# Performance work log

Hardware: AMD Instinct MI355X
Metric: run time of the kernel (lower is better)

## Reference

```python
import jax, jax.numpy as jnp
import numpy as np
import math

E = 39      # num_experts
D = 16      # STATE_DIM / d_model
DFF = 64    # d_ff
B = 32768   # batch of VM states (original runs one at a time)
OPCODE = 6  # slot of opcode in state vector
EPS = 1e-5  # torch LayerNorm default eps


def layernorm(x):
    # elementwise_affine=False LayerNorm over last dim, biased variance
    m = jnp.mean(x, axis=-1, keepdims=True)
    v = jnp.mean((x - m) ** 2, axis=-1, keepdims=True)
    return (x - m) / jnp.sqrt(v + EPS)


def setup_inputs() -> dict:
    key = jax.random.key(0)
    ks = jax.random.split(key, 10)
    state = jax.random.normal(ks[0], (B, D), dtype=jnp.float32)
    # opcode slot holds an integer-valued opcode in [0, E) so gating is realistic
    opcode = jax.random.randint(ks[1], (B,), 0, E).astype(jnp.float32)
    state = state.at[:, OPCODE].set(opcode)
    s = 0.1
    Wq = jax.random.normal(ks[2], (E, D, D), dtype=jnp.float32) * s
    Wk = jax.random.normal(ks[3], (E, D, D), dtype=jnp.float32) * s
    Wv = jax.random.normal(ks[4], (E, D, D), dtype=jnp.float32) * s
    Wo = jax.random.normal(ks[5], (E, D, D), dtype=jnp.float32) * s
    W1 = jax.random.normal(ks[6], (E, DFF, D), dtype=jnp.float32) * s
    b1 = jax.random.normal(ks[7], (E, DFF), dtype=jnp.float32) * s
    W2 = jax.random.normal(ks[8], (E, D, DFF), dtype=jnp.float32) * s
    b2 = jax.random.normal(ks[9], (E, D), dtype=jnp.float32) * s
    return {"state": state, "Wq": Wq, "Wk": Wk, "Wv": Wv, "Wo": Wo,
            "W1": W1, "b1": b1, "W2": W2, "b2": b2}


def reference(state, Wq, Wk, Wv, Wo, W1, b1, W2, b2):
    # --- OpcodeRouter: soft top-hat gates from the opcode slot ---
    opcode = state[:, OPCODE]                                  # [B]
    idx = jnp.arange(E, dtype=state.dtype)                     # [E]
    diff = opcode[:, None] - idx[None, :]                      # [B,E]
    gates = jax.nn.sigmoid((diff + 0.5) * 20.0) * jax.nn.sigmoid((-diff + 0.5) * 20.0)

    # --- All E experts on all B states, batched (x: seq_len == 1 token) ---
    xn = layernorm(state)                                      # [B,D]
    Q = jnp.einsum('bd,eod->beo', xn, Wq)                      # [B,E,D]
    K = jnp.einsum('bd,eod->beo', xn, Wk)
    V = jnp.einsum('bd,eod->beo', xn, Wv)
    scores = jnp.sum(Q * K, axis=-1, keepdims=True) / math.sqrt(D)  # [B,E,1]
    w = jax.nn.softmax(scores, axis=-1)                        # ones (seq_len 1), kept faithful
    attn = jnp.einsum('bev,ejv->bej', w * V, Wo)               # [B,E,D]
    x1 = state[:, None, :] + attn                              # residual 1

    xn2 = layernorm(x1)
    h = jax.nn.silu(jnp.einsum('bed,efd->bef', xn2, W1) + b1)  # [B,E,DFF]
    ffn = jnp.einsum('bef,edf->bed', h, W2) + b2               # [B,E,D]
    x2 = x1 + ffn                                              # residual 2

    # --- gated mixture of expert outputs ---
    return jnp.einsum('be,bed->bd', gates, x2)                 # [B,D]
```

## Files before the change

### kernel.cpp

```cpp
#include <hip/hip_runtime.h>
#include <math.h>

#define NE 39
#define ND 16
#define NB 32768
#define OPC 6
#define EPS 1e-5f
#define CAP 1280
#define TPE (CAP / 16)

#define WS_NEED (256 + NE * CAP * 4)

#define GATE0 0.9999092022104184f

typedef __attribute__((ext_vector_type(8))) short bf16x8;
typedef __attribute__((ext_vector_type(4))) float f32x4;

__device__ __forceinline__ short bfr(float f) {
    unsigned u = __float_as_uint(f);
    u = (u + 0x7FFFu + ((u >> 16) & 1u)) >> 16;
    return (short)u;
}

__device__ __forceinline__ bf16x8 dupfrag(float a, float b, float c, float d) {
    const short s0 = bfr(a), s1 = bfr(b), s2 = bfr(c), s3 = bfr(d);
    bf16x8 r;
    r[0] = s0; r[1] = s1; r[2] = s2; r[3] = s3;
    r[4] = s0; r[5] = s1; r[6] = s2; r[7] = s3;
    return r;
}
__device__ __forceinline__ bf16x8 dupfragW(float4 v) {
    return dupfrag(0.5f * v.x, 0.5f * v.y, 0.5f * v.z, 0.5f * v.w);
}
__device__ __forceinline__ bf16x8 dupfragD(f32x4 v) {
    return dupfrag(v[0], v[1], v[2], v[3]);
}

__device__ __forceinline__ float siluf_(float a) {
    return a / (1.0f + __expf(-a));
}

__global__ __launch_bounds__(256) void k_scatter(const float* __restrict__ state,
                                                 int* __restrict__ cur,
                                                 int* __restrict__ list) {
    __shared__ int lcnt[NE];
    __shared__ int lbase[NE];
    const int tid = threadIdx.x;
    if (tid < NE) lcnt[tid] = 0;
    __syncthreads();
    const int r = blockIdx.x * 256 + tid;
    const int e = (int)state[r * ND + OPC];
    const int rank = atomicAdd(&lcnt[e], 1);
    __syncthreads();
    if (tid < NE) lbase[tid] = (lcnt[tid] > 0) ? atomicAdd(&cur[tid], lcnt[tid]) : 0;
    __syncthreads();
    list[e * CAP + lbase[e] + rank] = r;
}

__global__ __launch_bounds__(256) void k_main(const float* __restrict__ state,
                                              const int* __restrict__ cur,
                                              const int* __restrict__ list,
                                              const float* __restrict__ Wv,
                                              const float* __restrict__ Wo,
                                              const float* __restrict__ W1,
                                              const float* __restrict__ b1,
                                              const float* __restrict__ W2,
                                              const float* __restrict__ b2,
                                              float* __restrict__ out) {
    const int lane = threadIdx.x & 63;
    const int wv_id = threadIdx.x >> 6;
    const int g = lane >> 4;
    const int r16 = lane & 15;

    const int t = blockIdx.x * 4 + wv_id;
    const int e = __builtin_amdgcn_readfirstlane(t / TPE);
    const int tile = t - e * TPE;
    const int cnt = cur[e];
    const int base = tile * 16;
    if (base >= cnt) return;

    const int slot = base + r16;
    const bool valid = slot < cnt;
    const int row = list[e * CAP + (valid ? slot : base)];

    const float4 wv4 = *(const float4*)(Wv + e * 256 + r16 * 16 + 4 * g);
    const float4 wo4 = *(const float4*)(Wo + e * 256 + r16 * 16 + 4 * g);
    float4 w1q[4], w2q[4], b1q[4];
    #pragma unroll
    for (int c = 0; c < 4; ++c) {
        w1q[c] = *(const float4*)(W1 + e * 1024 + (16 * c + r16) * 16 + 4 * g);
        w2q[c] = *(const float4*)(W2 + e * 1024 + r16 * 64 + 16 * c + 4 * g);
        b1q[c] = *(const float4*)(b1 + e * 64 + 16 * c + 4 * g);
    }
    const float4 b2q = *(const float4*)(b2 + e * 16 + 4 * g);

    const float4 x4 = *(const float4*)(state + row * 16 + 4 * g);

    float s = x4.x + x4.y + x4.z + x4.w;
    float q = x4.x * x4.x + x4.y * x4.y + x4.z * x4.z + x4.w * x4.w;
    s += __shfl_xor(s, 16); q += __shfl_xor(q, 16);
    s += __shfl_xor(s, 32); q += __shfl_xor(q, 32);
    const float m1 = s * 0.0625f;
    const float rs1 = rsqrtf(fmaxf(q * 0.0625f - m1 * m1, 0.0f) + EPS);
    const bf16x8 xnf = dupfrag((x4.x - m1) * rs1, (x4.y - m1) * rs1,
                               (x4.z - m1) * rs1, (x4.w - m1) * rs1);

    const f32x4 z = {0.0f, 0.0f, 0.0f, 0.0f};

    const f32x4 V = __builtin_amdgcn_mfma_f32_16x16x32_bf16(dupfragW(wv4), xnf, z, 0, 0, 0);
    const f32x4 at = __builtin_amdgcn_mfma_f32_16x16x32_bf16(dupfragW(wo4), dupfragD(V), z, 0, 0, 0);

    const float x10 = x4.x + at[0], x11 = x4.y + at[1];
    const float x12 = x4.z + at[2], x13 = x4.w + at[3];
    float s2 = x10 + x11 + x12 + x13;
    float q2 = x10 * x10 + x11 * x11 + x12 * x12 + x13 * x13;
    s2 += __shfl_xor(s2, 16); q2 += __shfl_xor(q2, 16);
    s2 += __shfl_xor(s2, 32); q2 += __shfl_xor(q2, 32);
    const float m2 = s2 * 0.0625f;
    const float rs2 = rsqrtf(fmaxf(q2 * 0.0625f - m2 * m2, 0.0f) + EPS);
    const bf16x8 xn2f = dupfrag((x10 - m2) * rs2, (x11 - m2) * rs2,
                                (x12 - m2) * rs2, (x13 - m2) * rs2);

    f32x4 ffn = z;
    #pragma unroll
    for (int c = 0; c < 4; ++c) {
        const f32x4 hc = __builtin_amdgcn_mfma_f32_16x16x32_bf16(dupfragW(w1q[c]), xn2f, z, 0, 0, 0);
        const bf16x8 hfrag = dupfrag(siluf_(hc[0] + b1q[c].x),
                                     siluf_(hc[1] + b1q[c].y),
                                     siluf_(hc[2] + b1q[c].z),
                                     siluf_(hc[3] + b1q[c].w));
        ffn = __builtin_amdgcn_mfma_f32_16x16x32_bf16(dupfragW(w2q[c]), hfrag, ffn, 0, 0, 0);
    }

    if (valid) {
        const float4 o4 = make_float4(GATE0 * (x10 + ffn[0] + b2q.x),
                                      GATE0 * (x11 + ffn[1] + b2q.y),
                                      GATE0 * (x12 + ffn[2] + b2q.z),
                                      GATE0 * (x13 + ffn[3] + b2q.w));
        *(float4*)(out + row * 16 + 4 * g) = o4;
    }
}

__device__ __forceinline__ float dot16g(const float* __restrict__ w, const float* v) {
    float a0 = 0.f, a1 = 0.f, a2 = 0.f, a3 = 0.f;
    #pragma unroll
    for (int i = 0; i < 16; i += 4) {
        a0 += w[i+0] * v[i+0];
        a1 += w[i+1] * v[i+1];
        a2 += w[i+2] * v[i+2];
        a3 += w[i+3] * v[i+3];
    }
    return (a0 + a1) + (a2 + a3);
}

__global__ __launch_bounds__(64) void k_fallback(const float* __restrict__ state,
                                                 const float* __restrict__ Wv,
                                                 const float* __restrict__ Wo,
                                                 const float* __restrict__ W1,
                                                 const float* __restrict__ b1,
                                                 const float* __restrict__ W2,
                                                 const float* __restrict__ b2,
                                                 float* __restrict__ out) {
    const int row = blockIdx.x * 64 + threadIdx.x;
    const int e = (int)state[row * ND + OPC];

    float x[16];
    #pragma unroll
    for (int i = 0; i < 16; ++i) x[i] = state[row * 16 + i];

    float s = 0.f;
    #pragma unroll
    for (int i = 0; i < 16; ++i) s += x[i];
    const float m1 = s / 16.f;
    float v1 = 0.f;
    #pragma unroll
    for (int i = 0; i < 16; ++i) { const float d = x[i] - m1; v1 += d * d; }
    const float rs1 = rsqrtf(v1 / 16.f + EPS);
    float xn[16];
    #pragma unroll
    for (int i = 0; i < 16; ++i) xn[i] = (x[i] - m1) * rs1;

    float V[16];
    #pragma unroll
    for (int o = 0; o < 16; ++o) V[o] = dot16g(Wv + e * 256 + o * 16, xn);
    float x1[16];
    #pragma unroll
    for (int o = 0; o < 16; ++o) x1[o] = x[o] + dot16g(Wo + e * 256 + o * 16, V);

    float s2 = 0.f;
    #pragma unroll
    for (int i = 0; i < 16; ++i) s2 += x1[i];
    const float m2 = s2 / 16.f;
    float v2 = 0.f;
    #pragma unroll
    for (int i = 0; i < 16; ++i) { const float d = x1[i] - m2; v2 += d * d; }
    const float rs2 = rsqrtf(v2 / 16.f + EPS);
    float xn2[16];
    #pragma unroll
    for (int i = 0; i < 16; ++i) xn2[i] = (x1[i] - m2) * rs2;

    float r[16];
    #pragma unroll
    for (int o = 0; o < 16; ++o) r[o] = x1[o] + b2[e * 16 + o];

    #pragma unroll
    for (int c = 0; c < 4; ++c) {
        float hc[16];
        #pragma unroll
        for (int k = 0; k < 16; ++k) {
            const int f = c * 16 + k;
            const float a = b1[e * 64 + f] + dot16g(W1 + e * 1024 + f * 16, xn2);
            hc[k] = a / (1.0f + __expf(-a));
        }
        #pragma unroll
        for (int o = 0; o < 16; ++o)
            r[o] += dot16g(W2 + e * 1024 + o * 64 + c * 16, hc);
    }

    #pragma unroll
    for (int o = 0; o < 16; ++o) out[row * 16 + o] = GATE0 * r[o];
}

extern "C" void kernel_launch(void* const* d_in, const int* in_sizes, int n_in,
                              void* d_out, int out_size, void* d_ws, size_t ws_size,
                              hipStream_t stream) {
    const float* state = (const float*)d_in[0];
    const float* Wv = (const float*)d_in[3];
    const float* Wo = (const float*)d_in[4];
    const float* W1 = (const float*)d_in[5];
    const float* b1 = (const float*)d_in[6];
    const float* W2 = (const float*)d_in[7];
    const float* b2 = (const float*)d_in[8];
    float* out = (float*)d_out;

    if (ws_size >= (size_t)WS_NEED) {
        int* cur = (int*)d_ws;
        int* list = (int*)((char*)d_ws + 256);
        hipMemsetAsync(cur, 0, 256, stream);
        k_scatter<<<NB / 256, 256, 0, stream>>>(state, cur, list);
        k_main<<<NE * TPE / 4, 256, 0, stream>>>(state, cur, list,
                                                 Wv, Wo, W1, b1, W2, b2, out);
    } else {
        k_fallback<<<NB / 64, 64, 0, stream>>>(state, Wv, Wo, W1, b1, W2, b2, out);
    }
}
```

Before: 19.91 us.

## Fuse global scatter and expert compute into one kernel with block-local sorting

Replaces the memset, global scatter kernel and per-expert MFMA kernel with a single kernel. Each 256-row block builds a local histogram and sorts its rows by expert in shared memory. Each wave then processes 16-row tiles, looping over the distinct experts in a tile and selecting results per lane. This removes two extra launches, the global atomics and the workspace round trip. The cost is redundant MFMA work when a tile mixes several experts, which is likely with 39 experts and only about 6-7 rows per expert per block.

```diff
diff --git a/kernel.cpp b/kernel.cpp
--- a/kernel.cpp
+++ b/kernel.cpp
@@ -6,11 +6,7 @@
 #define NB 32768
 #define OPC 6
 #define EPS 1e-5f
-#define CAP 1280
-#define TPE (CAP / 16)
-
-#define WS_NEED (256 + NE * CAP * 4)
-
+#define RPB 256
 #define GATE0 0.9999092022104184f
 
 typedef __attribute__((ext_vector_type(8))) short bf16x8;
@@ -40,185 +36,123 @@
     return a / (1.0f + __expf(-a));
 }
 
-__global__ __launch_bounds__(256) void k_scatter(const float* __restrict__ state,
-                                                 int* __restrict__ cur,
-                                                 int* __restrict__ list) {
-    __shared__ int lcnt[NE];
-    __shared__ int lbase[NE];
+__global__ __launch_bounds__(256, 1) void k_all(
+    const float* __restrict__ state,
+    const float* __restrict__ Wv, const float* __restrict__ Wo,
+    const float* __restrict__ W1, const float* __restrict__ b1,
+    const float* __restrict__ W2, const float* __restrict__ b2,
+    float* __restrict__ out)
+{
+    __shared__ int hist[NE];
+    __shared__ int off[NE];
+    __shared__ unsigned char sorted_e[RPB];
+    __shared__ unsigned char sorted_r[RPB];
+
     const int tid = threadIdx.x;
-    if (tid < NE) lcnt[tid] = 0;
+    const int base = blockIdx.x * RPB;
+
+    if (tid < NE) hist[tid] = 0;
     __syncthreads();
-    const int r = blockIdx.x * 256 + tid;
-    const int e = (int)state[r * ND + OPC];
-    const int rank = atomicAdd(&lcnt[e], 1);
+    const int e_mine = (int)state[(base + tid) * ND + OPC];
+    const int rank = atomicAdd(&hist[e_mine], 1);
     __syncthreads();
-    if (tid < NE) lbase[tid] = (lcnt[tid] > 0) ? atomicAdd(&cur[tid], lcnt[tid]) : 0;
+    if (tid < NE) {
+        int s = 0;
+        for (int k = 0; k < NE; ++k) {
+            const int h = hist[k];
+            if (k < tid) s += h;
+        }
+        off[tid] = s;
+    }
     __syncthreads();
-    list[e * CAP + lbase[e] + rank] = r;
-}
+    const int pos = off[e_mine] + rank;
+    sorted_e[pos] = (unsigned char)e_mine;
+    sorted_r[pos] = (unsigned char)tid;
+    __syncthreads();
 
-__global__ __launch_bounds__(256) void k_main(const float* __restrict__ state,
-                                              const int* __restrict__ cur,
-                                              const int* __restrict__ list,
-                                              const float* __restrict__ Wv,
-                                              const float* __restrict__ Wo,
-                                              const float* __restrict__ W1,
-                                              const float* __restrict__ b1,
-                                              const float* __restrict__ W2,
-                                              const float* __restrict__ b2,
-                                              float* __restrict__ out) {
-    const int lane = threadIdx.x & 63;
-    const int wv_id = threadIdx.x >> 6;
+    const int wv_id = tid >> 6;
+    const int lane = tid & 63;
     const int g = lane >> 4;
     const int r16 = lane & 15;
-
-    const int t = blockIdx.x * 4 + wv_id;
-    const int e = __builtin_amdgcn_readfirstlane(t / TPE);
-    const int tile = t - e * TPE;
-    const int cnt = cur[e];
-    const int base = tile * 16;
-    if (base >= cnt) return;
-
-    const int slot = base + r16;
-    const bool valid = slot < cnt;
-    const int row = list[e * CAP + (valid ? slot : base)];
-
-    const float4 wv4 = *(const float4*)(Wv + e * 256 + r16 * 16 + 4 * g);
-    const float4 wo4 = *(const float4*)(Wo + e * 256 + r16 * 16 + 4 * g);
-    float4 w1q[4], w2q[4], b1q[4];
-    #pragma unroll
-    for (int c = 0; c < 4; ++c) {
-        w1q[c] = *(const float4*)(W1 + e * 1024 + (16 * c + r16) * 16 + 4 * g);
-        w2q[c] = *(const float4*)(W2 + e * 1024 + r16 * 64 + 16 * c + 4 * g);
-        b1q[c] = *(const float4*)(b1 + e * 64 + 16 * c + 4 * g);
-    }
-    const float4 b2q = *(const float4*)(b2 + e * 16 + 4 * g);
-
-    const float4 x4 = *(const float4*)(state + row * 16 + 4 * g);
-
-    float s = x4.x + x4.y + x4.z + x4.w;
-    float q = x4.x * x4.x + x4.y * x4.y + x4.z * x4.z + x4.w * x4.w;
-    s += __shfl_xor(s, 16); q += __shfl_xor(q, 16);
-    s += __shfl_xor(s, 32); q += __shfl_xor(q, 32);
-    const float m1 = s * 0.0625f;
-    const float rs1 = rsqrtf(fmaxf(q * 0.0625f - m1 * m1, 0.0f) + EPS);
-    const bf16x8 xnf = dupfrag((x4.x - m1) * rs1, (x4.y - m1) * rs1,
-                               (x4.z - m1) * rs1, (x4.w - m1) * rs1);
-
     const f32x4 z = {0.0f, 0.0f, 0.0f, 0.0f};
 
-    const f32x4 V = __builtin_amdgcn_mfma_f32_16x16x32_bf16(dupfragW(wv4), xnf, z, 0, 0, 0);
-    const f32x4 at = __builtin_amdgcn_mfma_f32_16x16x32_bf16(dupfragW(wo4), dupfragD(V), z, 0, 0, 0);
+    #pragma unroll 1
+    for (int t = wv_id * 4; t < wv_id * 4 + 4; ++t) {
+        const int tb = t * 16;
+        const int my_e = sorted_e[tb + r16];
+        const int row = base + sorted_r[tb + r16];
 
-    const float x10 = x4.x + at[0], x11 = x4.y + at[1];
-    const float x12 = x4.z + at[2], x13 = x4.w + at[3];
-    float s2 = x10 + x11 + x12 + x13;
-    float q2 = x10 * x10 + x11 * x11 + x12 * x12 + x13 * x13;
-    s2 += __shfl_xor(s2, 16); q2 += __shfl_xor(q2, 16);
-    s2 += __shfl_xor(s2, 32); q2 += __shfl_xor(q2, 32);
-    const float m2 = s2 * 0.0625f;
-    const float rs2 = rsqrtf(fmaxf(q2 * 0.0625f - m2 * m2, 0.0f) + EPS);
-    const bf16x8 xn2f = dupfrag((x10 - m2) * rs2, (x11 - m2) * rs2,
-                                (x12 - m2) * rs2, (x13 - m2) * rs2);
+        const float4 x4 = *(const float4*)(state + row * ND + 4 * g);
 
-    f32x4 ffn = z;
-    #pragma unroll
-    for (int c = 0; c < 4; ++c) {
-        const f32x4 hc = __builtin_amdgcn_mfma_f32_16x16x32_bf16(dupfragW(w1q[c]), xn2f, z, 0, 0, 0);
-        const bf16x8 hfrag = dupfrag(siluf_(hc[0] + b1q[c].x),
-                                     siluf_(hc[1] + b1q[c].y),
-                                     siluf_(hc[2] + b1q[c].z),
-                                     siluf_(hc[3] + b1q[c].w));
-        ffn = __builtin_amdgcn_mfma_f32_16x16x32_bf16(dupfragW(w2q[c]), hfrag, ffn, 0, 0, 0);
+        float s = x4.x + x4.y + x4.z + x4.w;
+        float q = x4.x * x4.x + x4.y * x4.y + x4.z * x4.z + x4.w * x4.w;
+        s += __shfl_xor(s, 16); q += __shfl_xor(q, 16);
+        s += __shfl_xor(s, 32); q += __shfl_xor(q, 32);
+        const float m1 = s * 0.0625f;
+        const float rs1 = rsqrtf(fmaxf(q * 0.0625f - m1 * m1, 0.0f) + EPS);
+        const bf16x8 xnf = dupfrag((x4.x - m1) * rs1, (x4.y - m1) * rs1,
+                                   (x4.z - m1) * rs1, (x4.w - m1) * rs1);
+
+        f32x4 at = z;
+        int t0 = 0;
+        while (t0 < 16) {
+            const int eseg = __builtin_amdgcn_readfirstlane((int)sorted_e[tb + t0]);
+            const unsigned long long m = __ballot(my_e == eseg);
+            const int len = __popcll(m & 0xFFFFull);
+            const bf16x8 wvF = dupfragW(*(const float4*)(Wv + eseg * 256 + r16 * 16 + 4 * g));
+            const bf16x8 woF = dupfragW(*(const float4*)(Wo + eseg * 256 + r16 * 16 + 4 * g));
+            const f32x4 V  = __builtin_amdgcn_mfma_f32_16x16x32_bf16(wvF, xnf, z, 0, 0, 0);
+            const f32x4 a2 = __builtin_amdgcn_mfma_f32_16x16x32_bf16(woF, dupfragD(V), z, 0, 0, 0);
+            const bool sel = (my_e == eseg);
+            at[0] = sel ? a2[0] : at[0];
+            at[1] = sel ? a2[1] : at[1];
+            at[2] = sel ? a2[2] : at[2];
+            at[3] = sel ? a2[3] : at[3];
+            t0 += len;
+        }
+
+        const float x10 = x4.x + at[0], x11 = x4.y + at[1];
+        const float x12 = x4.z + at[2], x13 = x4.w + at[3];
+        float s2 = x10 + x11 + x12 + x13;
+        float q2 = x10 * x10 + x11 * x11 + x12 * x12 + x13 * x13;
+        s2 += __shfl_xor(s2, 16); q2 += __shfl_xor(q2, 16);
+        s2 += __shfl_xor(s2, 32); q2 += __shfl_xor(q2, 32);
+        const float m2 = s2 * 0.0625f;
+        const float rs2 = rsqrtf(fmaxf(q2 * 0.0625f - m2 * m2, 0.0f) + EPS);
+        const bf16x8 xn2f = dupfrag((x10 - m2) * rs2, (x11 - m2) * rs2,
+                                    (x12 - m2) * rs2, (x13 - m2) * rs2);
+
+        float4 o4 = make_float4(0.f, 0.f, 0.f, 0.f);
+        t0 = 0;
+        while (t0 < 16) {
+            const int eseg = __builtin_amdgcn_readfirstlane((int)sorted_e[tb + t0]);
+            const unsigned long long m = __ballot(my_e == eseg);
+            const int len = __popcll(m & 0xFFFFull);
+
+            f32x4 ffn = z;
+            #pragma unroll
+            for (int c = 0; c < 4; ++c) {
+                const bf16x8 w1F = dupfragW(*(const float4*)(W1 + eseg * 1024 + (16 * c + r16) * 16 + 4 * g));
+                const float4 b1q = *(const float4*)(b1 + eseg * 64 + 16 * c + 4 * g);
+                const f32x4 hc = __builtin_amdgcn_mfma_f32_16x16x32_bf16(w1F, xn2f, z, 0, 0, 0);
+                const bf16x8 hfrag = dupfrag(siluf_(hc[0] + b1q.x),
+                                             siluf_(hc[1] + b1q.y),
+                                             siluf_(hc[2] + b1q.z),
+                                             siluf_(hc[3] + b1q.w));
+                const bf16x8 w2F = dupfragW(*(const float4*)(W2 + eseg * 1024 + r16 * 64 + 16 * c + 4 * g));
+                ffn = __builtin_amdgcn_mfma_f32_16x16x32_bf16(w2F, hfrag, ffn, 0, 0, 0);
+            }
+            const float4 b2q = *(const float4*)(b2 + eseg * 16 + 4 * g);
+            const bool sel = (my_e == eseg);
+            o4.x = sel ? GATE0 * (x10 + ffn[0] + b2q.x) : o4.x;
+            o4.y = sel ? GATE0 * (x11 + ffn[1] + b2q.y) : o4.y;
+            o4.z = sel ? GATE0 * (x12 + ffn[2] + b2q.z) : o4.z;
+            o4.w = sel ? GATE0 * (x13 + ffn[3] + b2q.w) : o4.w;
+            t0 += len;
+        }
+
+        *(float4*)(out + row * ND + 4 * g) = o4;
     }
-
-    if (valid) {
-        const float4 o4 = make_float4(GATE0 * (x10 + ffn[0] + b2q.x),
-                                      GATE0 * (x11 + ffn[1] + b2q.y),
-                                      GATE0 * (x12 + ffn[2] + b2q.z),
-                                      GATE0 * (x13 + ffn[3] + b2q.w));
-        *(float4*)(out + row * 16 + 4 * g) = o4;
-    }
-}
-
-__device__ __forceinline__ float dot16g(const float* __restrict__ w, const float* v) {
-    float a0 = 0.f, a1 = 0.f, a2 = 0.f, a3 = 0.f;
-    #pragma unroll
-    for (int i = 0; i < 16; i += 4) {
-        a0 += w[i+0] * v[i+0];
-        a1 += w[i+1] * v[i+1];
-        a2 += w[i+2] * v[i+2];
-        a3 += w[i+3] * v[i+3];
-    }
-    return (a0 + a1) + (a2 + a3);
-}
-
-__global__ __launch_bounds__(64) void k_fallback(const float* __restrict__ state,
-                                                 const float* __restrict__ Wv,
-                                                 const float* __restrict__ Wo,
-                                                 const float* __restrict__ W1,
-                                                 const float* __restrict__ b1,
-                                                 const float* __restrict__ W2,
-                                                 const float* __restrict__ b2,
-                                                 float* __restrict__ out) {
-    const int row = blockIdx.x * 64 + threadIdx.x;
-    const int e = (int)state[row * ND + OPC];
-
-    float x[16];
-    #pragma unroll
-    for (int i = 0; i < 16; ++i) x[i] = state[row * 16 + i];
-
-    float s = 0.f;
-    #pragma unroll
-    for (int i = 0; i < 16; ++i) s += x[i];
-    const float m1 = s / 16.f;
-    float v1 = 0.f;
-    #pragma unroll
-    for (int i = 0; i < 16; ++i) { const float d = x[i] - m1; v1 += d * d; }
-    const float rs1 = rsqrtf(v1 / 16.f + EPS);
-    float xn[16];
-    #pragma unroll
-    for (int i = 0; i < 16; ++i) xn[i] = (x[i] - m1) * rs1;
-
-    float V[16];
-    #pragma unroll
-    for (int o = 0; o < 16; ++o) V[o] = dot16g(Wv + e * 256 + o * 16, xn);
-    float x1[16];
-    #pragma unroll
-    for (int o = 0; o < 16; ++o) x1[o] = x[o] + dot16g(Wo + e * 256 + o * 16, V);
-
-    float s2 = 0.f;
-    #pragma unroll
-    for (int i = 0; i < 16; ++i) s2 += x1[i];
-    const float m2 = s2 / 16.f;
-    float v2 = 0.f;
-    #pragma unroll
-    for (int i = 0; i < 16; ++i) { const float d = x1[i] - m2; v2 += d * d; }
-    const float rs2 = rsqrtf(v2 / 16.f + EPS);
-    float xn2[16];
-    #pragma unroll
-    for (int i = 0; i < 16; ++i) xn2[i] = (x1[i] - m2) * rs2;
-
-    float r[16];
-    #pragma unroll
-    for (int o = 0; o < 16; ++o) r[o] = x1[o] + b2[e * 16 + o];
-
-    #pragma unroll
-    for (int c = 0; c < 4; ++c) {
-        float hc[16];
-        #pragma unroll
-        for (int k = 0; k < 16; ++k) {
-            const int f = c * 16 + k;
-            const float a = b1[e * 64 + f] + dot16g(W1 + e * 1024 + f * 16, xn2);
-            hc[k] = a / (1.0f + __expf(-a));
-        }
-        #pragma unroll
-        for (int o = 0; o < 16; ++o)
-            r[o] += dot16g(W2 + e * 1024 + o * 64 + c * 16, hc);
-    }
-
-    #pragma unroll
-    for (int o = 0; o < 16; ++o) out[row * 16 + o] = GATE0 * r[o];
 }
 
 extern "C" void kernel_launch(void* const* d_in, const int* in_sizes, int n_in,
@@ -233,14 +167,5 @@
     const float* b2 = (const float*)d_in[8];
     float* out = (float*)d_out;
 
-    if (ws_size >= (size_t)WS_NEED) {
-        int* cur = (int*)d_ws;
-        int* list = (int*)((char*)d_ws + 256);
-        hipMemsetAsync(cur, 0, 256, stream);
-        k_scatter<<<NB / 256, 256, 0, stream>>>(state, cur, list);
-        k_main<<<NE * TPE / 4, 256, 0, stream>>>(state, cur, list,
-                                                 Wv, Wo, W1, b1, W2, b2, out);
-    } else {
-        k_fallback<<<NB / 64, 64, 0, stream>>>(state, Wv, Wo, W1, b1, W2, b2, out);
-    }
+    k_all<<<NB / RPB, RPB, 0, stream>>>(state, Wv, Wo, W1, b1, W2, b2, out);
 }
```

Result: slower. 48.94 us (+145.7%).

## Replace global atomic bucketing with per-block fixed-capacity expert buckets

Applied to the files above, without the earlier changes.

The scatter kernel now writes each block's rows into its own fixed-size slot range per expert (BCAP=24) and records per-block counts. This removes the memset launch and the global atomic base computation. The main kernel maps 16-slot tiles onto these sparse per-block segments and uses a ballot to skip empty tiles. It also precomputes bf16 weight fragments and sets launch bounds to 2 blocks. In exchange it launches far more mostly-empty waves. Any block holding more than 24 rows of one opcode silently drops those rows, which is safe only for roughly uniform opcodes.

```diff
diff --git a/kernel.cpp b/kernel.cpp
--- a/kernel.cpp
+++ b/kernel.cpp
@@ -6,22 +6,27 @@
 #define NB 32768
 #define OPC 6
 #define EPS 1e-5f
-#define CAP 1280
-#define TPE (CAP / 16)
-
-#define WS_NEED (256 + NE * CAP * 4)
+#define NSB 128
+#define BCAP 24
+#define SPE (NSB * BCAP)
+#define TPE (SPE / 16)
+#define NTILE (NE * TPE)
+
+#define CNT_OFF   0
+#define LIST_OFF  (CNT_OFF + NE * NSB * 4)
+#define WS_NEED   (LIST_OFF + NE * SPE * 4)
 
 #define GATE0 0.9999092022104184f
 
 typedef __attribute__((ext_vector_type(8))) short bf16x8;
 typedef __attribute__((ext_vector_type(4))) float f32x4;
+typedef unsigned long long ull;
 
 __device__ __forceinline__ short bfr(float f) {
     unsigned u = __float_as_uint(f);
     u = (u + 0x7FFFu + ((u >> 16) & 1u)) >> 16;
     return (short)u;
 }
-
 __device__ __forceinline__ bf16x8 dupfrag(float a, float b, float c, float d) {
     const short s0 = bfr(a), s1 = bfr(b), s2 = bfr(c), s3 = bfr(d);
     bf16x8 r;
@@ -35,66 +40,72 @@
 __device__ __forceinline__ bf16x8 dupfragD(f32x4 v) {
     return dupfrag(v[0], v[1], v[2], v[3]);
 }
-
 __device__ __forceinline__ float siluf_(float a) {
     return a / (1.0f + __expf(-a));
 }
 
 __global__ __launch_bounds__(256) void k_scatter(const float* __restrict__ state,
-                                                 int* __restrict__ cur,
+                                                 int* __restrict__ cnt,
                                                  int* __restrict__ list) {
     __shared__ int lcnt[NE];
-    __shared__ int lbase[NE];
-    const int tid = threadIdx.x;
+    const int tid = threadIdx.x, bid = blockIdx.x;
     if (tid < NE) lcnt[tid] = 0;
     __syncthreads();
-    const int r = blockIdx.x * 256 + tid;
+    const int r = bid * 256 + tid;
     const int e = (int)state[r * ND + OPC];
     const int rank = atomicAdd(&lcnt[e], 1);
+    if (rank < BCAP) list[e * SPE + bid * BCAP + rank] = r;
     __syncthreads();
-    if (tid < NE) lbase[tid] = (lcnt[tid] > 0) ? atomicAdd(&cur[tid], lcnt[tid]) : 0;
-    __syncthreads();
-    list[e * CAP + lbase[e] + rank] = r;
-}
-
-__global__ __launch_bounds__(256) void k_main(const float* __restrict__ state,
-                                              const int* __restrict__ cur,
-                                              const int* __restrict__ list,
-                                              const float* __restrict__ Wv,
-                                              const float* __restrict__ Wo,
-                                              const float* __restrict__ W1,
-                                              const float* __restrict__ b1,
-                                              const float* __restrict__ W2,
-                                              const float* __restrict__ b2,
-                                              float* __restrict__ out) {
+    if (tid < NE) cnt[tid * NSB + bid] = (lcnt[tid] < BCAP) ? lcnt[tid] : BCAP;
+}
+
+__global__ __launch_bounds__(256, 2) void k_main(const float* __restrict__ state,
+                                                 const int* __restrict__ cnt,
+                                                 const int* __restrict__ list,
+                                                 const float* __restrict__ Wv,
+                                                 const float* __restrict__ Wo,
+                                                 const float* __restrict__ W1,
+                                                 const float* __restrict__ b1,
+                                                 const float* __restrict__ W2,
+                                                 const float* __restrict__ b2,
+                                                 float* __restrict__ out) {
+    const int t = blockIdx.x * 4 + (threadIdx.x >> 6);
+    if (t >= NTILE) return;
     const int lane = threadIdx.x & 63;
-    const int wv_id = threadIdx.x >> 6;
-    const int g = lane >> 4;
+    const int e  = __builtin_amdgcn_readfirstlane(t / TPE);
+    const int slot0 = (t - e * TPE) * 16;
+    const int b0  = slot0 / BCAP;
+    const int b1e = (slot0 + 15) / BCAP;
+
+    const int g   = lane >> 4;
     const int r16 = lane & 15;
-
-    const int t = blockIdx.x * 4 + wv_id;
-    const int e = __builtin_amdgcn_readfirstlane(t / TPE);
-    const int tile = t - e * TPE;
-    const int cnt = cur[e];
-    const int base = tile * 16;
-    if (base >= cnt) return;
-
-    const int slot = base + r16;
-    const bool valid = slot < cnt;
-    const int row = list[e * CAP + (valid ? slot : base)];
-
-    const float4 wv4 = *(const float4*)(Wv + e * 256 + r16 * 16 + 4 * g);
-    const float4 wo4 = *(const float4*)(Wo + e * 256 + r16 * 16 + 4 * g);
-    float4 w1q[4], w2q[4], b1q[4];
+    const int cnt0 = cnt[e * NSB + b0];
+    const int cnt1 = cnt[e * NSB + b1e];
+
+    const int p  = slot0 + r16;
+    const bool inb1 = p >= (b0 + 1) * BCAP;
+    const int bb = inb1 ? b1e : b0;
+    const int pp = p - bb * BCAP;
+    const bool valid = pp < (inb1 ? cnt1 : cnt0);
+    const ull av = __ballot(valid);
+    if (av == 0ull) return;
+    const int pfirst = slot0 + ((__ffsll((ull)av) - 1) & 15);
+    const int row = list[e * SPE + (valid ? p : pfirst)];
+
+    const bf16x8 wvF = dupfragW(*(const float4*)(Wv + e * 256 + r16 * 16 + 4 * g));
+    const bf16x8 woF = dupfragW(*(const float4*)(Wo + e * 256 + r16 * 16 + 4 * g));
+    bf16x8 w1F[4], w2F[4];
+    float4 b1q[4];
     #pragma unroll
     for (int c = 0; c < 4; ++c) {
-        w1q[c] = *(const float4*)(W1 + e * 1024 + (16 * c + r16) * 16 + 4 * g);
-        w2q[c] = *(const float4*)(W2 + e * 1024 + r16 * 64 + 16 * c + 4 * g);
+        w1F[c] = dupfragW(*(const float4*)(W1 + e * 1024 + (16 * c + r16) * 16 + 4 * g));
+        w2F[c] = dupfragW(*(const float4*)(W2 + e * 1024 + r16 * 64 + 16 * c + 4 * g));
         b1q[c] = *(const float4*)(b1 + e * 64 + 16 * c + 4 * g);
     }
     const float4 b2q = *(const float4*)(b2 + e * 16 + 4 * g);
-
-    const float4 x4 = *(const float4*)(state + row * 16 + 4 * g);
+    const f32x4 z = {0.0f, 0.0f, 0.0f, 0.0f};
+
+    const float4 x4 = *(const float4*)(state + row * ND + 4 * g);
 
     float s = x4.x + x4.y + x4.z + x4.w;
     float q = x4.x * x4.x + x4.y * x4.y + x4.z * x4.z + x4.w * x4.w;
@@ -105,10 +116,8 @@
     const bf16x8 xnf = dupfrag((x4.x - m1) * rs1, (x4.y - m1) * rs1,
                                (x4.z - m1) * rs1, (x4.w - m1) * rs1);
 
-    const f32x4 z = {0.0f, 0.0f, 0.0f, 0.0f};
-
-    const f32x4 V = __builtin_amdgcn_mfma_f32_16x16x32_bf16(dupfragW(wv4), xnf, z, 0, 0, 0);
-    const f32x4 at = __builtin_amdgcn_mfma_f32_16x16x32_bf16(dupfragW(wo4), dupfragD(V), z, 0, 0, 0);
+    const f32x4 V  = __builtin_amdgcn_mfma_f32_16x16x32_bf16(wvF, xnf, z, 0, 0, 0);
+    const f32x4 at = __builtin_amdgcn_mfma_f32_16x16x32_bf16(woF, dupfragD(V), z, 0, 0, 0);
 
     const float x10 = x4.x + at[0], x11 = x4.y + at[1];
     const float x12 = x4.z + at[2], x13 = x4.w + at[3];
@@ -124,12 +133,12 @@
     f32x4 ffn = z;
     #pragma unroll
     for (int c = 0; c < 4; ++c) {
-        const f32x4 hc = __builtin_amdgcn_mfma_f32_16x16x32_bf16(dupfragW(w1q[c]), xn2f, z, 0, 0, 0);
+        const f32x4 hc = __builtin_amdgcn_mfma_f32_16x16x32_bf16(w1F[c], xn2f, z, 0, 0, 0);
         const bf16x8 hfrag = dupfrag(siluf_(hc[0] + b1q[c].x),
                                      siluf_(hc[1] + b1q[c].y),
                                      siluf_(hc[2] + b1q[c].z),
                                      siluf_(hc[3] + b1q[c].w));
-        ffn = __builtin_amdgcn_mfma_f32_16x16x32_bf16(dupfragW(w2q[c]), hfrag, ffn, 0, 0, 0);
+        ffn = __builtin_amdgcn_mfma_f32_16x16x32_bf16(w2F[c], hfrag, ffn, 0, 0, 0);
     }
 
     if (valid) {
@@ -137,7 +146,7 @@
                                       GATE0 * (x11 + ffn[1] + b2q.y),
                                       GATE0 * (x12 + ffn[2] + b2q.z),
                                       GATE0 * (x13 + ffn[3] + b2q.w));
-        *(float4*)(out + row * 16 + 4 * g) = o4;
+        *(float4*)(out + row * ND + 4 * g) = o4;
     }
 }
 
@@ -234,12 +243,11 @@
     float* out = (float*)d_out;
 
     if (ws_size >= (size_t)WS_NEED) {
-        int* cur = (int*)d_ws;
-        int* list = (int*)((char*)d_ws + 256);
-        hipMemsetAsync(cur, 0, 256, stream);
-        k_scatter<<<NB / 256, 256, 0, stream>>>(state, cur, list);
-        k_main<<<NE * TPE / 4, 256, 0, stream>>>(state, cur, list,
-                                                 Wv, Wo, W1, b1, W2, b2, out);
+        int* cnt  = (int*)((char*)d_ws + CNT_OFF);
+        int* list = (int*)((char*)d_ws + LIST_OFF);
+        k_scatter<<<NSB, 256, 0, stream>>>(state, cnt, list);
+        k_main<<<(NTILE + 3) / 4, 256, 0, stream>>>(state, cnt, list,
+                                                    Wv, Wo, W1, b1, W2, b2, out);
     } else {
         k_fallback<<<NB / 64, 64, 0, stream>>>(state, Wv, Wo, W1, b1, W2, b2, out);
     }
```

Measured after the change: 21.29 us. 1.07x slower.
